# Kernel tuning notes

Hardware: AMD Instinct MI355X
Metric: run time of the kernel (lower is better)

Reference implementation:

```python
import jax, jax.numpy as jnp
import numpy as np

# Config matching init_kwargs (single TP rank: local heads == total heads)
HID = 1024
NH = 16      # query heads
NKV = 4      # kv heads (GQA)
HD = 64      # head_dim
B = 2
S = 2048
SCALE = 1.0 / HD ** 0.5


def setup_inputs() -> dict:
    key = jax.random.key(0)
    k1, k2, k3 = jax.random.split(key, 3)
    qkv_out = (NH + 2 * NKV) * HD  # 1536
    return {
        "hidden_states": jax.random.normal(k1, (B, S, HID), dtype=jnp.float32),
        "W_qkv": jax.random.normal(k2, (HID, qkv_out), dtype=jnp.float32) * 0.02,
        "W_o": jax.random.normal(k3, (HID, HID), dtype=jnp.float32) * 0.02,
    }


def reference(hidden_states, W_qkv, W_o):
    b, s, _ = hidden_states.shape
    rep = NH // NKV  # GQA repeat factor (repeat_interleave: q head h uses kv group h // rep)

    qkv = hidden_states @ W_qkv  # [B, S, (NH+2*NKV)*HD]
    q, k, v = jnp.split(qkv, [NH * HD, (NH + NKV) * HD], axis=-1)

    # [B, heads, S, HD]
    q = q.reshape(b, s, NH, HD).transpose(0, 2, 1, 3)
    k = k.reshape(b, s, NKV, HD).transpose(0, 2, 1, 3)
    v = v.reshape(b, s, NKV, HD).transpose(0, 2, 1, 3)

    # Group query heads by shared kv head instead of repeat_interleaving K/V in memory.
    qg = q.reshape(b, NKV, rep, s, HD)  # head h = g*rep + r  <=>  kv group g = h // rep
    scores = jnp.einsum("bgrqd,bgkd->bgrqk", qg, k) * SCALE  # [B, NKV, rep, S, S]

    # Causal mask (prefill path: kv_cache is None, seq_len > 1)
    causal = jnp.triu(jnp.ones((s, s), dtype=bool), k=1)
    scores = jnp.where(causal, jnp.finfo(scores.dtype).min, scores)

    attn = jax.nn.softmax(scores, axis=-1)
    out = jnp.einsum("bgrqk,bgkd->bgrqd", attn, v)  # [B, NKV, rep, S, HD]
    out = out.reshape(b, NH, s, HD).transpose(0, 2, 1, 3).reshape(b, s, NH * HD)
    return out @ W_o  # [B, S, HID]
```

## Files before the change

### kernel.cpp

```cpp
#include <hip/hip_runtime.h>
#include <stdint.h>

using u16 = unsigned short;
using u32 = unsigned int;

typedef __attribute__((ext_vector_type(8))) short short8;
typedef __attribute__((ext_vector_type(4))) float f32x4;
typedef __attribute__((ext_vector_type(16))) float f32x16;

__device__ __forceinline__ u16 f2bf(float f) {
  u32 u = __builtin_bit_cast(u32, f);
  u = (u + 0x7fffu + ((u >> 16) & 1u)) >> 16;
  return (u16)u;
}

__device__ __forceinline__ u32 cvtpk(float lo, float hi) {
  u32 r;
  asm("v_cvt_pk_bf16_f32 %0, %1, %2" : "=v"(r) : "v"(lo), "v"(hi));
  return r;
}

__device__ __forceinline__ short8 ld16(const u16* p) {
  uint4 v = *(const uint4*)p;
  union { uint4 u; short8 s; } c; c.u = v; return c.s;
}

__device__ __forceinline__ void gload_lds16(const void* g, void* l) {
  __builtin_amdgcn_global_load_lds(
      (const __attribute__((address_space(1))) void*)g,
      (__attribute__((address_space(3))) void*)l, 16, 0, 0);
}

__device__ __forceinline__ f32x16 mfma32(short8 a, short8 b, f32x16 c) {
  return __builtin_amdgcn_mfma_f32_32x32x16_bf16(a, b, c, 0, 0, 0);
}

__global__ __launch_bounds__(256) void k_prep(const float* __restrict__ hs,
                                              const float* __restrict__ wqkv,
                                              const float* __restrict__ wo,
                                              u16* __restrict__ hsb,
                                              u16* __restrict__ wqkvT,
                                              u16* __restrict__ woT) {
  __shared__ float tile[32][33];
  const int bid = blockIdx.x;
  if (bid < 4096) {
    int i = bid * 256 + threadIdx.x;
    float4 v = ((const float4*)hs)[i];
    ushort4 o;
    o.x = f2bf(v.x); o.y = f2bf(v.y); o.z = f2bf(v.z); o.w = f2bf(v.w);
    ((ushort4*)hsb)[i] = o;
    return;
  }
  const float* in; u16* out; int R, C, bx, by;
  if (bid < 5632) {
    int idx = bid - 4096;
    in = wqkv; out = wqkvT; R = 1024; C = 1536;
    bx = idx % 48; by = idx / 48;
  } else {
    int idx = bid - 5632;
    in = wo; out = woT; R = 1024; C = 1024;
    bx = idx & 31; by = idx >> 5;
  }
  int c0 = bx * 32, r0 = by * 32;
  int tx = threadIdx.x & 31, ty = threadIdx.x >> 5;
#pragma unroll
  for (int i = 0; i < 4; ++i) {
    int r = ty + 8 * i;
    tile[r][tx] = in[(size_t)(r0 + r) * C + c0 + tx];
  }
  __syncthreads();
#pragma unroll
  for (int i = 0; i < 4; ++i) {
    int r = ty + 8 * i;
    out[(size_t)(c0 + r) * R + r0 + tx] = f2bf(tile[tx][r]);
  }
}

__global__ __launch_bounds__(256, 3) void k_gemm_qkv(
    const u16* __restrict__ A, const u16* __restrict__ BT,
    u16* __restrict__ qb, u16* __restrict__ kb, u16* __restrict__ vbT) {
  const int K = 1024;
  __shared__ __align__(16) u16 As[2][64 * 64];
  __shared__ __align__(16) u16 Bs[2][128 * 64];
  const int t = threadIdx.x;
  const int l = t & 63;
  const int wid = t >> 6;
  const int wr = wid >> 1, wc = wid & 1;
  const int lr = l & 15, lg = l >> 4;
  const int cpx = (int)gridDim.x >> 3;
  const int nb = (blockIdx.x & 7) * cpx + ((int)blockIdx.x >> 3);
  const int mt = nb / 12, nt = nb % 12;
  const int m0 = mt << 6, n0 = nt << 7;

  f32x4 zero = {0.f, 0.f, 0.f, 0.f};
  f32x4 acc[2][4];
#pragma unroll
  for (int i = 0; i < 2; ++i)
#pragma unroll
    for (int j = 0; j < 4; ++j) acc[i][j] = zero;

  const u16* Ab = A + (size_t)m0 * K;
  const u16* Bb = BT + (size_t)n0 * K;

  auto STAGE = [&](int kt, int bsel) {
    const u16* Ak = Ab + kt * 64;
    const u16* Bk = Bb + kt * 64;
#pragma unroll
    for (int i = 0; i < 2; ++i) {
      int o16 = i * 256 + t;
      int row = o16 >> 3, c = o16 & 7;
      int sc = c ^ (row & 7);
      gload_lds16(Ak + (size_t)row * K + sc * 8, &As[bsel][o16 * 8]);
    }
#pragma unroll
    for (int i = 0; i < 4; ++i) {
      int o16 = i * 256 + t;
      int row = o16 >> 3, c = o16 & 7;
      int sc = c ^ (row & 7);
      gload_lds16(Bk + (size_t)row * K + sc * 8, &Bs[bsel][o16 * 8]);
    }
  };

  STAGE(0, 0);
  asm volatile("s_waitcnt vmcnt(0)" ::: "memory");
  __builtin_amdgcn_s_barrier();

  for (int kt = 0; kt < 16; ++kt) {
    const int cur = kt & 1;
    if (kt + 1 < 16) STAGE(kt + 1, cur ^ 1);
#pragma unroll
    for (int ks = 0; ks < 2; ++ks) {
      short8 a[2], b[4];
#pragma unroll
      for (int mi = 0; mi < 2; ++mi) {
        int row = wr * 32 + mi * 16 + lr;
        int c = (ks * 4 + lg) ^ (row & 7);
        a[mi] = ld16(&As[cur][(row * 8 + c) * 8]);
      }
#pragma unroll
      for (int ni = 0; ni < 4; ++ni) {
        int row = wc * 64 + ni * 16 + lr;
        int c = (ks * 4 + lg) ^ (row & 7);
        b[ni] = ld16(&Bs[cur][(row * 8 + c) * 8]);
      }
#pragma unroll
      for (int mi = 0; mi < 2; ++mi)
#pragma unroll
        for (int ni = 0; ni < 4; ++ni)
          acc[mi][ni] = __builtin_amdgcn_mfma_f32_16x16x32_bf16(a[mi], b[ni], acc[mi][ni], 0, 0, 0);
    }
    asm volatile("s_waitcnt vmcnt(0)" ::: "memory");
    __builtin_amdgcn_s_barrier();
    asm volatile("" ::: "memory");
  }

#pragma unroll
  for (int mi = 0; mi < 2; ++mi) {
#pragma unroll
    for (int ni = 0; ni < 4; ++ni) {
#pragma unroll
      for (int r = 0; r < 4; ++r) {
        float v = acc[mi][ni][r];
        int m = m0 + wr * 32 + mi * 16 + 4 * lg + r;
        int n = n0 + wc * 64 + ni * 16 + lr;
        int bb = m >> 11, s = m & 2047;
        int tau = s >> 5, i32e = s & 31;
        if (n < 1024) {
          int h = n >> 6, d = n & 63;
          int kc = d >> 4, hi2 = (d >> 3) & 1, e = d & 7;
          qb[((size_t)(bb * 16 + h)) * 131072 +
             (size_t)((tau * 4 + kc) * 64 + (hi2 << 5 | i32e)) * 8 + e] = f2bf(v * 0.18033688f);
        } else if (n < 1280) {
          int g = (n - 1024) >> 6, d = n & 63;
          int kc = d >> 4, hi2 = (d >> 3) & 1, e = d & 7;
          kb[((size_t)(bb * 4 + g)) * 131072 +
             (size_t)((tau * 4 + kc) * 64 + (hi2 << 5 | i32e)) * 8 + e] = f2bf(v);
        } else {
          int g = (n - 1280) >> 6, dT = n & 63;
          int c = (s >> 4) & 1, hi2 = (s >> 3) & 1, e = s & 7;
          int dd = dT >> 5, i32v = dT & 31;
          vbT[((size_t)(bb * 4 + g)) * 131072 +
              (size_t)(((tau * 2 + dd) * 2 + c) * 64 + (hi2 << 5 | i32v)) * 8 + e] = f2bf(v);
        }
      }
    }
  }
}

__global__ __launch_bounds__(256, 2) void k_gemm_out(
    const u16* __restrict__ A, const u16* __restrict__ BT, float* __restrict__ out) {
  const int K = 1024, N = 1024;
  __shared__ __align__(16) u16 As[2][64 * 64];
  __shared__ __align__(16) u16 Bs[2][128 * 64];
  const int t = threadIdx.x;
  const int l = t & 63;
  const int wid = t >> 6;
  const int wr = wid >> 1, wc = wid & 1;
  const int lr = l & 15, lg = l >> 4;
  const int cpx = (int)gridDim.x >> 3;
  const int nb = (blockIdx.x & 7) * cpx + ((int)blockIdx.x >> 3);
  const int mt = nb >> 3, nt = nb & 7;
  const int m0 = mt << 6, n0 = nt << 7;

  f32x4 zero = {0.f, 0.f, 0.f, 0.f};
  f32x4 acc[2][4];
#pragma unroll
  for (int i = 0; i < 2; ++i)
#pragma unroll
    for (int j = 0; j < 4; ++j) acc[i][j] = zero;

  const u16* Ab = A + (size_t)m0 * K;
  const u16* Bb = BT + (size_t)n0 * K;

  auto STAGE = [&](int kt, int bsel) {
    const u16* Ak = Ab + kt * 64;
    const u16* Bk = Bb + kt * 64;
#pragma unroll
    for (int i = 0; i < 2; ++i) {
      int o16 = i * 256 + t;
      int row = o16 >> 3, c = o16 & 7;
      int sc = c ^ (row & 7);
      gload_lds16(Ak + (size_t)row * K + sc * 8, &As[bsel][o16 * 8]);
    }
#pragma unroll
    for (int i = 0; i < 4; ++i) {
      int o16 = i * 256 + t;
      int row = o16 >> 3, c = o16 & 7;
      int sc = c ^ (row & 7);
      gload_lds16(Bk + (size_t)row * K + sc * 8, &Bs[bsel][o16 * 8]);
    }
  };

  STAGE(0, 0);
  asm volatile("s_waitcnt vmcnt(0)" ::: "memory");
  __builtin_amdgcn_s_barrier();

  for (int kt = 0; kt < 16; ++kt) {
    const int cur = kt & 1;
    if (kt + 1 < 16) STAGE(kt + 1, cur ^ 1);
#pragma unroll
    for (int ks = 0; ks < 2; ++ks) {
      short8 a[2], b[4];
#pragma unroll
      for (int mi = 0; mi < 2; ++mi) {
        int row = wr * 32 + mi * 16 + lr;
        int c = (ks * 4 + lg) ^ (row & 7);
        a[mi] = ld16(&As[cur][(row * 8 + c) * 8]);
      }
#pragma unroll
      for (int ni = 0; ni < 4; ++ni) {
        int row = wc * 64 + ni * 16 + lr;
        int c = (ks * 4 + lg) ^ (row & 7);
        b[ni] = ld16(&Bs[cur][(row * 8 + c) * 8]);
      }
#pragma unroll
      for (int mi = 0; mi < 2; ++mi)
#pragma unroll
        for (int ni = 0; ni < 4; ++ni)
          acc[mi][ni] = __builtin_amdgcn_mfma_f32_16x16x32_bf16(a[mi], b[ni], acc[mi][ni], 0, 0, 0);
    }
    asm volatile("s_waitcnt vmcnt(0)" ::: "memory");
    __builtin_amdgcn_s_barrier();
    asm volatile("" ::: "memory");
  }

#pragma unroll
  for (int mi = 0; mi < 2; ++mi)
#pragma unroll
    for (int ni = 0; ni < 4; ++ni)
#pragma unroll
      for (int r = 0; r < 4; ++r) {
        int m = m0 + wr * 32 + mi * 16 + 4 * lg + r;
        int n = n0 + wc * 64 + ni * 16 + lr;
        out[(size_t)m * N + n] = acc[mi][ni][r];
      }
}

__global__ __launch_bounds__(256, 2) void k_attn(const u16* __restrict__ qbuf,
                                                 const u16* __restrict__ kbuf,
                                                 const u16* __restrict__ vbuf,
                                                 u16* __restrict__ attn) {
  __shared__ float osh[2][2048];
  __shared__ float lsh[2][64];
  const int t = threadIdx.x;
  const int l = t & 63, wid = t >> 6;
  const int i32 = l & 31, hi = l >> 5;
  const int bh = blockIdx.x >> 5;
  const int j = blockIdx.x & 31;
  const int b = bh >> 4, h = bh & 15, g = h >> 2;
  const int slot = wid >> 1, w01 = wid & 1;
  const int qt = (slot == 0) ? j : 63 - j;
  const int q0 = qt * 32;
  const int nblk = (qt >> 1) + 1;

  const u16* qp = qbuf + ((size_t)(b * 16 + h)) * 131072;
  const u16* kp = kbuf + ((size_t)(b * 4 + g)) * 131072;
  const u16* vp = vbuf + ((size_t)(b * 4 + g)) * 131072;

  short8 qf[4];
#pragma unroll
  for (int kc = 0; kc < 4; ++kc)
    qf[kc] = ld16(qp + ((size_t)((q0 >> 5) * 4 + kc) * 64 + l) * 8);

  f32x16 z16 = {0.f, 0.f, 0.f, 0.f, 0.f, 0.f, 0.f, 0.f,
                0.f, 0.f, 0.f, 0.f, 0.f, 0.f, 0.f, 0.f};
  f32x16 o[2];
  o[0] = z16; o[1] = z16;
  float lsum = 0.f;

  short8 kA[2][4], kB[2][4];

  auto LOADK = [&](short8(&kf)[2][4], int kv0) {
#pragma unroll
    for (int mf = 0; mf < 2; ++mf)
#pragma unroll
      for (int kc = 0; kc < 4; ++kc)
        kf[mf][kc] = ld16(kp + ((size_t)((((kv0 >> 5) + mf) * 4 + kc)) * 64 + l) * 8);
  };

  auto PROCESS = [&](short8(&kf)[2][4], short8(&kn)[2][4], bool pref, int kv0, bool last) {
    short8 vf[2][2][2];
#pragma unroll
    for (int mf = 0; mf < 2; ++mf)
#pragma unroll
      for (int dd = 0; dd < 2; ++dd)
#pragma unroll
        for (int c = 0; c < 2; ++c)
          vf[dd][mf][c] = ld16(vp + ((size_t)((((kv0 >> 5) + mf) * 2 + dd) * 2 + c) * 64 + l) * 8);

    f32x16 sc[2];
    __builtin_amdgcn_s_setprio(1);
    sc[0] = mfma32(kf[0][0], qf[0], z16);
    sc[1] = mfma32(kf[1][0], qf[0], z16);
#pragma unroll
    for (int kc = 1; kc < 4; ++kc) {
      sc[0] = mfma32(kf[0][kc], qf[kc], sc[0]);
      sc[1] = mfma32(kf[1][kc], qf[kc], sc[1]);
    }
    __builtin_amdgcn_s_setprio(0);

    if (pref) LOADK(kn, kv0 + 128);

    if (last) {
      const int iloc = (q0 - kv0) + i32;
#pragma unroll
      for (int mf = 0; mf < 2; ++mf)
#pragma unroll
        for (int R = 0; R < 16; ++R) {
          int j2 = 32 * mf + (R & 3) + 8 * (R >> 2) + 4 * hi;
          if (j2 > iloc) sc[mf][R] = -1e30f;
        }
    }

    float s0 = 0.f, s1 = 0.f, s2 = 0.f, s3 = 0.f;
#pragma unroll
    for (int mf = 0; mf < 2; ++mf)
#pragma unroll
      for (int R = 0; R < 16; R += 4) {
        float p0 = __builtin_amdgcn_exp2f(sc[mf][R]);
        float p1 = __builtin_amdgcn_exp2f(sc[mf][R + 1]);
        float p2 = __builtin_amdgcn_exp2f(sc[mf][R + 2]);
        float p3 = __builtin_amdgcn_exp2f(sc[mf][R + 3]);
        sc[mf][R] = p0; sc[mf][R + 1] = p1; sc[mf][R + 2] = p2; sc[mf][R + 3] = p3;
        s0 += p0; s1 += p1; s2 += p2; s3 += p3;
      }
    lsum += (s0 + s1) + (s2 + s3);

    short8 pb[2][2];
#pragma unroll
    for (int mf = 0; mf < 2; ++mf)
#pragma unroll
      for (int c = 0; c < 2; ++c) {
        union { u32 w[4]; short8 s8; } U;
#pragma unroll
        for (int q = 0; q < 2; ++q) {
          u32 wa = cvtpk(sc[mf][8 * c + 2 * q], sc[mf][8 * c + 2 * q + 1]);
          u32 wb = cvtpk(sc[mf][8 * c + 4 + 2 * q], sc[mf][8 * c + 4 + 2 * q + 1]);
          auto rr = __builtin_amdgcn_permlane32_swap(wa, wb, false, false);
          U.w[q] = (u32)rr[0];
          U.w[2 + q] = (u32)rr[1];
        }
        pb[mf][c] = U.s8;
      }

    __builtin_amdgcn_s_setprio(1);
#pragma unroll
    for (int mf = 0; mf < 2; ++mf)
#pragma unroll
      for (int c = 0; c < 2; ++c) {
        o[0] = mfma32(vf[0][mf][c], pb[mf][c], o[0]);
        o[1] = mfma32(vf[1][mf][c], pb[mf][c], o[1]);
      }
    __builtin_amdgcn_s_setprio(0);
  };

  int n = w01;
  if (n < nblk) {
    LOADK(kA, n * 64);
    while (true) {
      PROCESS(kA, kB, n + 2 < nblk, n * 64, n == nblk - 1);
      n += 2; if (n >= nblk) break;
      PROCESS(kB, kA, n + 2 < nblk, n * 64, n == nblk - 1);
      n += 2; if (n >= nblk) break;
    }
  }

  if (w01 == 1) {
    float* dst = &osh[slot][0];
#pragma unroll
    for (int dd = 0; dd < 2; ++dd) {
      float4* d4 = (float4*)&dst[(dd * 64 + l) * 16];
#pragma unroll
      for (int q = 0; q < 4; ++q) {
        float4 v4;
        v4.x = o[dd][4 * q]; v4.y = o[dd][4 * q + 1];
        v4.z = o[dd][4 * q + 2]; v4.w = o[dd][4 * q + 3];
        d4[q] = v4;
      }
    }
    lsh[slot][l] = lsum;
  }
  __syncthreads();
  if (w01 == 0) {
    const float* src = &osh[slot][0];
#pragma unroll
    for (int dd = 0; dd < 2; ++dd) {
      const float4* s4 = (const float4*)&src[(dd * 64 + l) * 16];
#pragma unroll
      for (int q = 0; q < 4; ++q) {
        float4 v4 = s4[q];
        o[dd][4 * q] += v4.x; o[dd][4 * q + 1] += v4.y;
        o[dd][4 * q + 2] += v4.z; o[dd][4 * q + 3] += v4.w;
      }
    }
    lsum += lsh[slot][l];

    float tot;
    {
      u32 su = __builtin_bit_cast(u32, lsum);
      auto rr = __builtin_amdgcn_permlane32_swap(su, su, false, false);
      tot = __builtin_bit_cast(float, (u32)rr[0]) + __builtin_bit_cast(float, (u32)rr[1]);
    }
    float inv = 1.f / tot;
    u16* ao = attn + ((size_t)(b * 2048 + q0)) * 1024 + h * 64;
#pragma unroll
    for (int dd = 0; dd < 2; ++dd) {
#pragma unroll
      for (int R = 0; R < 16; R += 2) {
        int d = dd * 32 + (R & 3) + 8 * (R >> 2) + 4 * hi;
        u32 w = cvtpk(o[dd][R] * inv, o[dd][R + 1] * inv);
        *(u32*)(ao + (size_t)i32 * 1024 + d) = w;
      }
    }
  }
}

extern "C" void kernel_launch(void* const* d_in, const int* in_sizes, int n_in,
                              void* d_out, int out_size, void* d_ws, size_t ws_size,
                              hipStream_t stream) {
  const float* hs = (const float*)d_in[0];
  const float* wqkv = (const float*)d_in[1];
  const float* wo = (const float*)d_in[2];
  float* out = (float*)d_out;
  u16* ws = (u16*)d_ws;

  u16* hsb = ws;
  u16* wqkvT = hsb + 4194304;
  u16* woT = wqkvT + 1572864;
  u16* qb = woT + 1048576;
  u16* kb = qb + 4194304;
  u16* vb = kb + 1048576;
  u16* attn = vb + 1048576;
  (void)in_sizes; (void)n_in; (void)out_size; (void)ws_size;

  k_prep<<<6656, 256, 0, stream>>>(hs, wqkv, wo, hsb, wqkvT, woT);
  k_gemm_qkv<<<768, 256, 0, stream>>>(hsb, wqkvT, qb, kb, vb);
  k_attn<<<1024, 256, 0, stream>>>(qb, kb, vb, attn);
  k_gemm_out<<<512, 256, 0, stream>>>(attn, woT, out);
}
```

Before: 88.70 us.

## Process two query tiles per K/V block in attention and rebalance causal work

Each wave now holds two adjacent 32-row query tiles and reuses every loaded K and V block for both, which halves K/V fetches per query row. Work is redistributed so each block takes a pair of short and long causal tile-pairs: wave 0 finishes the short pair and then part of the long pair, and wave 1 does the rest of the long pair; partial results are merged through shared memory. The grid shrinks from 1024 to 256 blocks with launch bounds of one block per SIMD group, so fewer waves are resident to hide latency and register pressure rises.

```diff
diff --git a/kernel.cpp b/kernel.cpp
--- a/kernel.cpp
+++ b/kernel.cpp
@@ -276,39 +276,41 @@
       }
 }
 
-__global__ __launch_bounds__(256, 2) void k_attn(const u16* __restrict__ qbuf,
+__global__ __launch_bounds__(256, 1) void k_attn(const u16* __restrict__ qbuf,
                                                  const u16* __restrict__ kbuf,
                                                  const u16* __restrict__ vbuf,
                                                  u16* __restrict__ attn) {
-  __shared__ float osh[2][2048];
-  __shared__ float lsh[2][64];
+  __shared__ float osh[2][4096];
+  __shared__ float lsh[2][128];
   const int t = threadIdx.x;
   const int l = t & 63, wid = t >> 6;
   const int i32 = l & 31, hi = l >> 5;
-  const int bh = blockIdx.x >> 5;
-  const int j = blockIdx.x & 31;
+  const int bh = blockIdx.x >> 3;
+  const int jj = blockIdx.x & 7;
   const int b = bh >> 4, h = bh & 15, g = h >> 2;
   const int slot = wid >> 1, w01 = wid & 1;
-  const int qt = (slot == 0) ? j : 63 - j;
-  const int q0 = qt * 32;
-  const int nblk = (qt >> 1) + 1;
+  const int cc = jj + slot * 8;
+  const int pA = cc, pB = 31 - cc;
+  const int split = 16 - cc;
 
   const u16* qp = qbuf + ((size_t)(b * 16 + h)) * 131072;
   const u16* kp = kbuf + ((size_t)(b * 4 + g)) * 131072;
   const u16* vp = vbuf + ((size_t)(b * 4 + g)) * 131072;
 
-  short8 qf[4];
-#pragma unroll
-  for (int kc = 0; kc < 4; ++kc)
-    qf[kc] = ld16(qp + ((size_t)((q0 >> 5) * 4 + kc) * 64 + l) * 8);
-
   f32x16 z16 = {0.f, 0.f, 0.f, 0.f, 0.f, 0.f, 0.f, 0.f,
                 0.f, 0.f, 0.f, 0.f, 0.f, 0.f, 0.f, 0.f};
-  f32x16 o[2];
-  o[0] = z16; o[1] = z16;
-  float lsum = 0.f;
-
+  short8 qfa[4], qfb[4];
+  f32x16 oa[2], ob[2];
+  float la, lb;
   short8 kA[2][4], kB[2][4];
+
+  auto LOADQ = [&](int p) {
+#pragma unroll
+    for (int kc = 0; kc < 4; ++kc) {
+      qfa[kc] = ld16(qp + ((size_t)((2 * p) * 4 + kc) * 64 + l) * 8);
+      qfb[kc] = ld16(qp + ((size_t)((2 * p + 1) * 4 + kc) * 64 + l) * 8);
+    }
+  };
 
   auto LOADK = [&](short8(&kf)[2][4], int kv0) {
 #pragma unroll
@@ -318,40 +320,17 @@
         kf[mf][kc] = ld16(kp + ((size_t)((((kv0 >> 5) + mf) * 4 + kc)) * 64 + l) * 8);
   };
 
-  auto PROCESS = [&](short8(&kf)[2][4], short8(&kn)[2][4], bool pref, int kv0, bool last) {
-    short8 vf[2][2][2];
-#pragma unroll
-    for (int mf = 0; mf < 2; ++mf)
-#pragma unroll
-      for (int dd = 0; dd < 2; ++dd)
-#pragma unroll
-        for (int c = 0; c < 2; ++c)
-          vf[dd][mf][c] = ld16(vp + ((size_t)((((kv0 >> 5) + mf) * 2 + dd) * 2 + c) * 64 + l) * 8);
-
-    f32x16 sc[2];
-    __builtin_amdgcn_s_setprio(1);
-    sc[0] = mfma32(kf[0][0], qf[0], z16);
-    sc[1] = mfma32(kf[1][0], qf[0], z16);
-#pragma unroll
-    for (int kc = 1; kc < 4; ++kc) {
-      sc[0] = mfma32(kf[0][kc], qf[kc], sc[0]);
-      sc[1] = mfma32(kf[1][kc], qf[kc], sc[1]);
-    }
-    __builtin_amdgcn_s_setprio(0);
-
-    if (pref) LOADK(kn, kv0 + 128);
-
-    if (last) {
-      const int iloc = (q0 - kv0) + i32;
+  auto SOFTPV = [&](f32x16(&sc)[2], short8(&vf)[2][2][2], f32x16(&o)[2], float& ls,
+                    bool dmask, int ilocb) {
+    if (dmask) {
 #pragma unroll
       for (int mf = 0; mf < 2; ++mf)
 #pragma unroll
         for (int R = 0; R < 16; ++R) {
           int j2 = 32 * mf + (R & 3) + 8 * (R >> 2) + 4 * hi;
-          if (j2 > iloc) sc[mf][R] = -1e30f;
+          if (j2 > ilocb + i32) sc[mf][R] = -1e30f;
         }
     }
-
     float s0 = 0.f, s1 = 0.f, s2 = 0.f, s3 = 0.f;
 #pragma unroll
     for (int mf = 0; mf < 2; ++mf)
@@ -364,8 +343,7 @@
         sc[mf][R] = p0; sc[mf][R + 1] = p1; sc[mf][R + 2] = p2; sc[mf][R + 3] = p3;
         s0 += p0; s1 += p1; s2 += p2; s3 += p3;
       }
-    lsum += (s0 + s1) + (s2 + s3);
-
+    ls += (s0 + s1) + (s2 + s3);
     short8 pb[2][2];
 #pragma unroll
     for (int mf = 0; mf < 2; ++mf)
@@ -382,7 +360,6 @@
         }
         pb[mf][c] = U.s8;
       }
-
     __builtin_amdgcn_s_setprio(1);
 #pragma unroll
     for (int mf = 0; mf < 2; ++mf)
@@ -394,64 +371,130 @@
     __builtin_amdgcn_s_setprio(0);
   };
 
-  int n = w01;
-  if (n < nblk) {
-    LOADK(kA, n * 64);
+  auto PROCESS = [&](short8(&kf)[2][4], short8(&kn)[2][4], bool pref, int n, int p) {
+    const int kv0 = n * 64;
+    short8 vf[2][2][2];
+#pragma unroll
+    for (int mf = 0; mf < 2; ++mf)
+#pragma unroll
+      for (int dd = 0; dd < 2; ++dd)
+#pragma unroll
+        for (int c = 0; c < 2; ++c)
+          vf[dd][mf][c] = ld16(vp + ((size_t)((((kv0 >> 5) + mf) * 2 + dd) * 2 + c) * 64 + l) * 8);
+
+    const bool dmask = (n == p);
+
+    f32x16 sc[2];
+    __builtin_amdgcn_s_setprio(1);
+    sc[0] = mfma32(kf[0][0], qfa[0], z16);
+    sc[1] = mfma32(kf[1][0], qfa[0], z16);
+#pragma unroll
+    for (int kc = 1; kc < 4; ++kc) {
+      sc[0] = mfma32(kf[0][kc], qfa[kc], sc[0]);
+      sc[1] = mfma32(kf[1][kc], qfa[kc], sc[1]);
+    }
+    __builtin_amdgcn_s_setprio(0);
+    if (pref) LOADK(kn, kv0 + 64);
+    SOFTPV(sc, vf, oa, la, dmask, 0);
+
+    f32x16 sd[2];
+    __builtin_amdgcn_s_setprio(1);
+    sd[0] = mfma32(kf[0][0], qfb[0], z16);
+    sd[1] = mfma32(kf[1][0], qfb[0], z16);
+#pragma unroll
+    for (int kc = 1; kc < 4; ++kc) {
+      sd[0] = mfma32(kf[0][kc], qfb[kc], sd[0]);
+      sd[1] = mfma32(kf[1][kc], qfb[kc], sd[1]);
+    }
+    __builtin_amdgcn_s_setprio(0);
+    SOFTPV(sd, vf, ob, lb, dmask, 32);
+  };
+
+  auto RUN = [&](int p, int n0, int n1) {
+    if (n0 >= n1) return;
+    LOADQ(p);
+    LOADK(kA, n0 * 64);
+    int n = n0;
     while (true) {
-      PROCESS(kA, kB, n + 2 < nblk, n * 64, n == nblk - 1);
-      n += 2; if (n >= nblk) break;
-      PROCESS(kB, kA, n + 2 < nblk, n * 64, n == nblk - 1);
-      n += 2; if (n >= nblk) break;
-    }
-  }
-
+      PROCESS(kA, kB, n + 1 < n1, n, p);
+      if (++n >= n1) break;
+      PROCESS(kB, kA, n + 1 < n1, n, p);
+      if (++n >= n1) break;
+    }
+  };
+
+  auto STOREPAIR = [&](int p) {
+#pragma unroll
+    for (int po = 0; po < 2; ++po) {
+      float ls = (po == 0) ? la : lb;
+      f32x16* o = (po == 0) ? oa : ob;
+      float tot;
+      {
+        u32 su = __builtin_bit_cast(u32, ls);
+        auto rr = __builtin_amdgcn_permlane32_swap(su, su, false, false);
+        tot = __builtin_bit_cast(float, (u32)rr[0]) + __builtin_bit_cast(float, (u32)rr[1]);
+      }
+      float inv = 1.f / tot;
+      u16* ao = attn + ((size_t)(b * 2048 + (2 * p + po) * 32)) * 1024 + h * 64;
+#pragma unroll
+      for (int dd = 0; dd < 2; ++dd) {
+#pragma unroll
+        for (int R = 0; R < 16; R += 2) {
+          int d = dd * 32 + (R & 3) + 8 * (R >> 2) + 4 * hi;
+          u32 w = cvtpk(o[dd][R] * inv, o[dd][R + 1] * inv);
+          *(u32*)(ao + (size_t)i32 * 1024 + d) = w;
+        }
+      }
+    }
+  };
+
+  oa[0] = z16; oa[1] = z16; ob[0] = z16; ob[1] = z16; la = 0.f; lb = 0.f;
+  if (w01 == 0) {
+    RUN(pA, 0, pA + 1);
+    STOREPAIR(pA);
+    oa[0] = z16; oa[1] = z16; ob[0] = z16; ob[1] = z16; la = 0.f; lb = 0.f;
+    RUN(pB, 0, split);
+    float* dst = &osh[slot][0];
+#pragma unroll
+    for (int po = 0; po < 2; ++po) {
+      f32x16* o = (po == 0) ? oa : ob;
+#pragma unroll
+      for (int dd = 0; dd < 2; ++dd) {
+        float4* d4 = (float4*)&dst[((po * 2 + dd) * 64 + l) * 16];
+#pragma unroll
+        for (int q = 0; q < 4; ++q) {
+          float4 v4;
+          v4.x = o[dd][4 * q]; v4.y = o[dd][4 * q + 1];
+          v4.z = o[dd][4 * q + 2]; v4.w = o[dd][4 * q + 3];
+          d4[q] = v4;
+        }
+      }
+    }
+    lsh[slot][l] = la;
+    lsh[slot][64 + l] = lb;
+  } else {
+    RUN(pB, split, pB + 1);
+  }
+  __syncthreads();
   if (w01 == 1) {
-    float* dst = &osh[slot][0];
-#pragma unroll
-    for (int dd = 0; dd < 2; ++dd) {
-      float4* d4 = (float4*)&dst[(dd * 64 + l) * 16];
-#pragma unroll
-      for (int q = 0; q < 4; ++q) {
-        float4 v4;
-        v4.x = o[dd][4 * q]; v4.y = o[dd][4 * q + 1];
-        v4.z = o[dd][4 * q + 2]; v4.w = o[dd][4 * q + 3];
-        d4[q] = v4;
-      }
-    }
-    lsh[slot][l] = lsum;
-  }
-  __syncthreads();
-  if (w01 == 0) {
     const float* src = &osh[slot][0];
 #pragma unroll
-    for (int dd = 0; dd < 2; ++dd) {
-      const float4* s4 = (const float4*)&src[(dd * 64 + l) * 16];
-#pragma unroll
-      for (int q = 0; q < 4; ++q) {
-        float4 v4 = s4[q];
-        o[dd][4 * q] += v4.x; o[dd][4 * q + 1] += v4.y;
-        o[dd][4 * q + 2] += v4.z; o[dd][4 * q + 3] += v4.w;
-      }
-    }
-    lsum += lsh[slot][l];
-
-    float tot;
-    {
-      u32 su = __builtin_bit_cast(u32, lsum);
-      auto rr = __builtin_amdgcn_permlane32_swap(su, su, false, false);
-      tot = __builtin_bit_cast(float, (u32)rr[0]) + __builtin_bit_cast(float, (u32)rr[1]);
-    }
-    float inv = 1.f / tot;
-    u16* ao = attn + ((size_t)(b * 2048 + q0)) * 1024 + h * 64;
-#pragma unroll
-    for (int dd = 0; dd < 2; ++dd) {
-#pragma unroll
-      for (int R = 0; R < 16; R += 2) {
-        int d = dd * 32 + (R & 3) + 8 * (R >> 2) + 4 * hi;
-        u32 w = cvtpk(o[dd][R] * inv, o[dd][R + 1] * inv);
-        *(u32*)(ao + (size_t)i32 * 1024 + d) = w;
-      }
-    }
+    for (int po = 0; po < 2; ++po) {
+      f32x16* o = (po == 0) ? oa : ob;
+#pragma unroll
+      for (int dd = 0; dd < 2; ++dd) {
+        const float4* s4 = (const float4*)&src[((po * 2 + dd) * 64 + l) * 16];
+#pragma unroll
+        for (int q = 0; q < 4; ++q) {
+          float4 v4 = s4[q];
+          o[dd][4 * q] += v4.x; o[dd][4 * q + 1] += v4.y;
+          o[dd][4 * q + 2] += v4.z; o[dd][4 * q + 3] += v4.w;
+        }
+      }
+    }
+    la += lsh[slot][l];
+    lb += lsh[slot][64 + l];
+    STOREPAIR(pB);
   }
 }
 
@@ -475,6 +518,6 @@
 
   k_prep<<<6656, 256, 0, stream>>>(hs, wqkv, wo, hsb, wqkvT, woT);
   k_gemm_qkv<<<768, 256, 0, stream>>>(hsb, wqkvT, qb, kb, vb);
-  k_attn<<<1024, 256, 0, stream>>>(qb, kb, vb, attn);
+  k_attn<<<256, 256, 0, stream>>>(qb, kb, vb, attn);
   k_gemm_out<<<512, 256, 0, stream>>>(attn, woT, out);
 }
```

Result: faster. 84.17 us, median of 3 (-5.1%).
